# Optimization experiments

Measured on AMD Instinct MI355X. Metric: run time of the kernel, lower is better.

Reference implementation:

```python
import jax, jax.numpy as jnp
import numpy as np

EPS = 1e-15
BN_EPS = 1e-5
N_NODES = 50000
N_EDGES = 800000
IN_CH = 32
OUT_CH = 32
DIM = 3


def _gmm_params(key, in_ch, out_ch, K):
    k1, k2, k3, k4 = jax.random.split(key, 4)
    g = jax.random.normal(k1, (in_ch, K * out_ch), jnp.float32) * (1.0 / np.sqrt(in_ch))
    mu = jax.random.normal(k2, (K, DIM), jnp.float32)
    sigma = jax.random.uniform(k3, (K, DIM), jnp.float32, 0.5, 1.5)
    root = jax.random.normal(k4, (in_ch, out_ch), jnp.float32) * (1.0 / np.sqrt(in_ch))
    bias = jnp.zeros((out_ch,), jnp.float32)
    return g, mu, sigma, root, bias


def setup_inputs() -> dict:
    key = jax.random.key(0)
    ks = jax.random.split(key, 12)
    x = jax.random.normal(ks[0], (N_NODES, IN_CH), jnp.float32)
    edge_index = jax.random.randint(ks[1], (2, N_EDGES), 0, N_NODES, jnp.int64)
    edge_attr = jax.random.uniform(ks[2], (N_EDGES, DIM), jnp.float32)
    g1, mu1, sig1, root1, b1 = _gmm_params(ks[3], IN_CH, OUT_CH, 5)
    g2, mu2, sig2, root2, b2 = _gmm_params(ks[4], OUT_CH, OUT_CH, 5)
    gs, mus, sigs, roots, bs = _gmm_params(ks[5], IN_CH, OUT_CH, 1)
    ones = jnp.ones((OUT_CH,), jnp.float32)
    zeros = jnp.zeros((OUT_CH,), jnp.float32)
    return dict(x=x, edge_attr=edge_attr,
                g1=g1, mu1=mu1, sig1=sig1, root1=root1, b1=b1, gam1=ones, bet1=zeros,
                g2=g2, mu2=mu2, sig2=sig2, root2=root2, b2=b2, gam2=ones, bet2=zeros,
                gs=gs, mus=mus, sigs=sigs, roots=roots, bs=bs, gams=ones, bets=zeros,
                edge_index=edge_index)


def gmm_conv(x, edge_index, edge_attr, g, mu, sigma, root, bias, num_nodes):
    # PyG GMMConv (separate kernels=False, aggr='mean', root_weight=True)
    src, dst = edge_index[0], edge_index[1]
    K = mu.shape[0]
    out_ch = root.shape[1]
    # Gaussian mixture weights per edge/kernel: [E, K]
    diff = edge_attr[:, None, :] - mu[None, :, :]               # [E, K, D]
    w = jnp.exp(jnp.sum(-0.5 * diff * diff / (EPS + sigma[None] ** 2), axis=-1))
    # Project and gather source features: [E, K, out]
    xj = (x @ g).reshape(-1, K, out_ch)[src] if False else (x[src] @ g).reshape(-1, K, out_ch)
    msg = jnp.einsum('ek,ekc->ec', w, xj)                        # [E, out]
    agg = jax.ops.segment_sum(msg, dst, num_segments=num_nodes)
    cnt = jax.ops.segment_sum(jnp.ones((msg.shape[0],), msg.dtype), dst, num_segments=num_nodes)
    agg = agg / jnp.maximum(cnt, 1.0)[:, None]                   # mean aggregation
    return agg + x @ root + bias


def batch_norm(x, gamma, beta):
    mean = jnp.mean(x, axis=0)
    var = jnp.var(x, axis=0)
    return gamma * (x - mean) * jax.lax.rsqrt(var + BN_EPS) + beta


def reference(x, edge_attr,
              g1, mu1, sig1, root1, b1, gam1, bet1,
              g2, mu2, sig2, root2, b2, gam2, bet2,
              gs, mus, sigs, roots, bs, gams, bets,
              edge_index):
    n = x.shape[0]
    h = jax.nn.elu(batch_norm(gmm_conv(x, edge_index, edge_attr, g1, mu1, sig1, root1, b1, n), gam1, bet1))
    h = batch_norm(gmm_conv(h, edge_index, edge_attr, g2, mu2, sig2, root2, b2, n), gam2, bet2)
    s = batch_norm(gmm_conv(x, edge_index, edge_attr, gs, mus, sigs, roots, bs, n), gams, bets)
    return jax.nn.elu(h + s)
```

## Files before the change

### kernel.cpp

```cpp
#include <hip/hip_runtime.h>
#include <hip/hip_fp16.h>
#include <math.h>

#define NN 50000
#define NE 800000
#define GEPS 1e-15f
#define BN_EPS 1e-5f
#define NB 196
#define LOG2E 1.4426950408889634f
#define NODES_PER_XCD 6250

typedef _Float16 f16x8 __attribute__((ext_vector_type(8)));
typedef float f32x4 __attribute__((ext_vector_type(4)));

__device__ __forceinline__ float2 h2f(unsigned int u) {
    __half2 h = *reinterpret_cast<const __half2*>(&u);
    return __half22float2(h);
}

__global__ void precompute_gc(const float* __restrict__ sig1, const float* __restrict__ mu1,
                              const float* __restrict__ sig2, const float* __restrict__ mu2,
                              const float* __restrict__ sigs, const float* __restrict__ mus,
                              float* __restrict__ gc) {
    int s = threadIdx.x;
    if (s >= 11) return;
    const float* sg; const float* mu;
    if (s < 5)       { sg = sig1 + s * 3;       mu = mu1 + s * 3; }
    else if (s < 10) { sg = sig2 + (s - 5) * 3; mu = mu2 + (s - 5) * 3; }
    else             { sg = sigs;               mu = mus; }
    float C = 0.f;
    for (int d = 0; d < 3; d++) {
        float sv = sg[d];
        float iv = -0.5f / (GEPS + sv * sv) * LOG2E;
        float m = mu[d];
        gc[s * 8 + d] = iv;
        gc[s * 8 + 3 + d] = -2.f * iv * m;
        C += iv * m * m;
    }
    gc[s * 8 + 6] = C;
    gc[s * 8 + 7] = 0.f;
}

__global__ void rank_kernel(const int* __restrict__ ei, int* __restrict__ deg,
                            int* __restrict__ rankv) {
    int t = blockIdx.x * blockDim.x + threadIdx.x;
    int e0 = t * 4;
    if (e0 >= NE) return;
    int4 dv = *(const int4*)(ei + NE + e0);
    int4 rv;
    rv.x = atomicAdd(&deg[dv.x], 1);
    rv.y = atomicAdd(&deg[dv.y], 1);
    rv.z = atomicAdd(&deg[dv.z], 1);
    rv.w = atomicAdd(&deg[dv.w], 1);
    *(int4*)(rankv + e0) = rv;
}

__global__ void block_reduce_kernel(const int* __restrict__ deg, int* __restrict__ bsum) {
    __shared__ int sh[256];
    int t = threadIdx.x;
    int i = blockIdx.x * 256 + t;
    sh[t] = (i < NN) ? deg[i] : 0;
    __syncthreads();
    for (int off = 128; off > 0; off >>= 1) {
        if (t < off) sh[t] += sh[t + off];
        __syncthreads();
    }
    if (t == 0) bsum[blockIdx.x] = sh[0];
}

__global__ void scan_partials_kernel(int* __restrict__ bsum) {
    __shared__ int sh[256];
    int t = threadIdx.x;
    int v = (t < NB) ? bsum[t] : 0;
    sh[t] = v;
    __syncthreads();
    for (int off = 1; off < 256; off <<= 1) {
        int u = (t >= off) ? sh[t - off] : 0;
        __syncthreads();
        sh[t] += u;
        __syncthreads();
    }
    if (t < NB) bsum[t] = sh[t] - v;
}

__global__ void block_scan_kernel(const int* __restrict__ deg, const int* __restrict__ bsum,
                                  int* __restrict__ rowstart) {
    __shared__ int sh[256];
    int t = threadIdx.x;
    int i = blockIdx.x * 256 + t;
    int v = (i < NN) ? deg[i] : 0;
    sh[t] = v;
    __syncthreads();
    for (int off = 1; off < 256; off <<= 1) {
        int u = (t >= off) ? sh[t - off] : 0;
        __syncthreads();
        sh[t] += u;
        __syncthreads();
    }
    int excl = sh[t] - v + bsum[blockIdx.x];
    if (i < NN) rowstart[i] = excl;
}

__global__ void scatter_xcd(const int* __restrict__ ei, const int* __restrict__ rankv,
                            const int* __restrict__ rowstart, int* __restrict__ perm) {
    const int g = blockIdx.x & 7;
    const int v = blockIdx.x >> 3;
    const int VB = gridDim.x >> 3;
    const int stride = VB * blockDim.x * 4;
    for (int e0 = (v * blockDim.x + threadIdx.x) * 4; e0 < NE; e0 += stride) {
        int4 dv = *(const int4*)(ei + NE + e0);
        int4 rv = *(const int4*)(rankv + e0);
        if (dv.x / NODES_PER_XCD == g) perm[rowstart[dv.x] + rv.x] = e0;
        if (dv.y / NODES_PER_XCD == g) perm[rowstart[dv.y] + rv.y] = e0 + 1;
        if (dv.z / NODES_PER_XCD == g) perm[rowstart[dv.z] + rv.z] = e0 + 2;
        if (dv.w / NODES_PER_XCD == g) perm[rowstart[dv.w] + rv.w] = e0 + 3;
    }
}

__global__ void reorder_build(const int* __restrict__ perm, const int* __restrict__ ei,
                              const float* __restrict__ ea, const float* __restrict__ gc,
                              int4* __restrict__ recA, int4* __restrict__ recB) {
    int t = blockIdx.x * blockDim.x + threadIdx.x;
    int p0 = t * 4;
    if (p0 >= NE) return;
    int4 pv = *(const int4*)(perm + p0);
    int es[4] = {pv.x, pv.y, pv.z, pv.w};

    int   srcs[4];
    float av[4][3];
#pragma unroll
    for (int k = 0; k < 4; k++) {
        int e = es[k];
        srcs[k] = ei[e];
        av[k][0] = ea[e * 3 + 0];
        av[k][1] = ea[e * 3 + 1];
        av[k][2] = ea[e * 3 + 2];
    }

    int4 qa[4], qb[4];
#pragma unroll
    for (int k = 0; k < 4; k++) {
        float a0 = av[k][0], a1 = av[k][1], a2 = av[k][2];
        float s0 = a0 * a0, s1 = a1 * a1, s2 = a2 * a2;
        __half wv[11];
#pragma unroll
        for (int s = 0; s < 11; s++) {
            float ex = gc[s * 8 + 6];
            ex = fmaf(gc[s * 8 + 3], a0, ex);
            ex = fmaf(gc[s * 8 + 4], a1, ex);
            ex = fmaf(gc[s * 8 + 5], a2, ex);
            ex = fmaf(gc[s * 8 + 0], s0, ex);
            ex = fmaf(gc[s * 8 + 1], s1, ex);
            ex = fmaf(gc[s * 8 + 2], s2, ex);
            wv[s] = __float2half(exp2f(ex));
        }
        union UA { struct { int src; __half w[6]; } r; int4 q; } ua;
        ua.r.src = srcs[k];
        ua.r.w[0] = wv[0]; ua.r.w[1] = wv[1]; ua.r.w[2] = wv[2];
        ua.r.w[3] = wv[3]; ua.r.w[4] = wv[4]; ua.r.w[5] = wv[10];
        union UB { struct { int src; __half w[5]; __half pad; } r; int4 q; } ub;
        ub.r.src = srcs[k];
        ub.r.w[0] = wv[5]; ub.r.w[1] = wv[6]; ub.r.w[2] = wv[7];
        ub.r.w[3] = wv[8]; ub.r.w[4] = wv[9]; ub.r.pad = __float2half(0.f);
        qa[k] = ua.q;
        qb[k] = ub.q;
    }
#pragma unroll
    for (int k = 0; k < 4; k++) recA[p0 + k] = qa[k];
#pragma unroll
    for (int k = 0; k < 4; k++) recB[p0 + k] = qb[k];
}

__global__ void projR_kernel(const float* __restrict__ x, const float* __restrict__ root1,
                             const float* __restrict__ b1, const float* __restrict__ roots,
                             const float* __restrict__ bs, __half* __restrict__ xh,
                             float* __restrict__ R1, float* __restrict__ Rs) {
    const int t = threadIdx.x;
    const int col = t & 31;
    const int half_ = (t >> 5) & 1;
    const int rg = t >> 6;
    float w[32];
    const float* rootp = half_ ? roots : root1;
#pragma unroll
    for (int i = 0; i < 32; i++) w[i] = rootp[i * 32 + col];
    float b = half_ ? bs[col] : b1[col];
    float* Rp = half_ ? Rs : R1;
    __shared__ float hs[256];
    for (int n0 = blockIdx.x * 8; n0 < NN; n0 += gridDim.x * 8) {
        float v = x[(size_t)n0 * 32 + t];
        hs[t] = v;
        xh[(size_t)n0 * 32 + t] = __float2half(v);
        __syncthreads();
#pragma unroll
        for (int rr = 0; rr < 2; rr++) {
            int r = rg * 2 + rr;
            float acc = b;
#pragma unroll
            for (int i = 0; i < 32; i++) acc += w[i] * hs[r * 32 + i];
            Rp[(size_t)(n0 + r) * 32 + col] = acc;
        }
        __syncthreads();
    }
}

__global__ void projB2_kernel(const float* __restrict__ c1, const float* __restrict__ stats,
                              const float* __restrict__ gam1, const float* __restrict__ bet1,
                              const float* __restrict__ root2, const float* __restrict__ b2,
                              __half* __restrict__ hh, float* __restrict__ R2) {
    const int t = threadIdx.x;
    const int col = t & 31;
    const int rg = t >> 5;
    __shared__ float sc[32], sf[32];
    if (t < 32) {
        const float invN = 1.0f / (float)NN;
        float m = stats[t] * invN;
        float v = stats[32 + t] * invN - m * m;
        float s = gam1[t] * rsqrtf(v + BN_EPS);
        sc[t] = s;
        sf[t] = bet1[t] - m * s;
    }
    float w[32];
#pragma unroll
    for (int i = 0; i < 32; i++) w[i] = root2[i * 32 + col];
    float b = b2[col];
    __shared__ float hs[256];
    __syncthreads();
    for (int n0 = blockIdx.x * 8; n0 < NN; n0 += gridDim.x * 8) {
        float v = c1[(size_t)n0 * 32 + t];
        float hv = sc[t & 31] * v + sf[t & 31];
        hv = hv > 0.f ? hv : (__expf(hv) - 1.f);
        hs[t] = hv;
        hh[(size_t)n0 * 32 + t] = __float2half(hv);
        __syncthreads();
        float acc = b;
#pragma unroll
        for (int i = 0; i < 32; i++) acc += w[i] * hs[rg * 32 + i];
        R2[(size_t)(n0 + rg) * 32 + col] = acc;
        __syncthreads();
    }
}

template <bool SKIP>
__global__ void agg_kernel(const int4* __restrict__ rec, const int* __restrict__ rowstart,
                           const int* __restrict__ deg, const __half* __restrict__ X,
                           __half* __restrict__ Aout) {
    constexpr int NS = SKIP ? 6 : 5;
    constexpr int SA = SKIP ? 192 : 160;
    const int tid = blockIdx.x * blockDim.x + threadIdx.x;
    const int lane = threadIdx.x & 63;
    const int grp = lane >> 4;
    const int ch2 = lane & 15;
    const int wavesTotal = (gridDim.x * blockDim.x) >> 6;
    const int wid = tid >> 6;

    for (int n = wid; n < NN; n += wavesTotal) {
        const int start = rowstart[n];
        const int d = deg[n];
        float2 acc[NS];
#pragma unroll
        for (int s = 0; s < NS; s++) acc[s] = make_float2(0.f, 0.f);
        int i = grp;
        for (; i + 4 < d; i += 8) {
            int4 r0 = rec[(size_t)(start + i)];
            int4 r1 = rec[(size_t)(start + i + 4)];
            const __half2 xv0 = *(const __half2*)(X + (((size_t)r0.x) << 5) + 2 * ch2);
            const __half2 xv1 = *(const __half2*)(X + (((size_t)r1.x) << 5) + 2 * ch2);
            float2 xf0 = __half22float2(xv0);
            float2 xf1 = __half22float2(xv1);
            {
                float2 w01 = h2f((unsigned)r0.y);
                float2 w23 = h2f((unsigned)r0.z);
                float2 w45 = h2f((unsigned)r0.w);
                float wv[6] = {w01.x, w01.y, w23.x, w23.y, w45.x, w45.y};
#pragma unroll
                for (int s = 0; s < NS; s++) {
                    acc[s].x = fmaf(wv[s], xf0.x, acc[s].x);
                    acc[s].y = fmaf(wv[s], xf0.y, acc[s].y);
                }
            }
            {
                float2 w01 = h2f((unsigned)r1.y);
                float2 w23 = h2f((unsigned)r1.z);
                float2 w45 = h2f((unsigned)r1.w);
                float wv[6] = {w01.x, w01.y, w23.x, w23.y, w45.x, w45.y};
#pragma unroll
                for (int s = 0; s < NS; s++) {
                    acc[s].x = fmaf(wv[s], xf1.x, acc[s].x);
                    acc[s].y = fmaf(wv[s], xf1.y, acc[s].y);
                }
            }
        }
        if (i < d) {
            int4 r = rec[(size_t)(start + i)];
            const __half2 xv = *(const __half2*)(X + (((size_t)r.x) << 5) + 2 * ch2);
            float2 xf = __half22float2(xv);
            float2 w01 = h2f((unsigned)r.y);
            float2 w23 = h2f((unsigned)r.z);
            float2 w45 = h2f((unsigned)r.w);
            float wv[6] = {w01.x, w01.y, w23.x, w23.y, w45.x, w45.y};
#pragma unroll
            for (int s = 0; s < NS; s++) {
                acc[s].x = fmaf(wv[s], xf.x, acc[s].x);
                acc[s].y = fmaf(wv[s], xf.y, acc[s].y);
            }
        }
#pragma unroll
        for (int s = 0; s < NS; s++) {
            acc[s].x += __shfl_xor(acc[s].x, 16, 64);
            acc[s].x += __shfl_xor(acc[s].x, 32, 64);
            acc[s].y += __shfl_xor(acc[s].y, 16, 64);
            acc[s].y += __shfl_xor(acc[s].y, 32, 64);
        }
        if (grp == 0) {
            const float invd = 1.0f / fmaxf((float)d, 1.0f);
            __half* base = Aout + (size_t)n * SA + 2 * ch2;
#pragma unroll
            for (int s = 0; s < 5; s++) {
                __half2 hv = __floats2half2_rn(acc[s].x * invd, acc[s].y * invd);
                *(__half2*)(base + s * 32) = hv;
            }
            if (SKIP) {
                __half2 hv = __floats2half2_rn(acc[5].x * invd, acc[5].y * invd);
                *(__half2*)(base + 160) = hv;
            }
        }
    }
}

template <bool SKIP>
__global__ __launch_bounds__(256, 4) void gemm_kernel(
        const __half* __restrict__ Ah, const float* __restrict__ G,
        const float* __restrict__ Gs, const float* __restrict__ R,
        const float* __restrict__ Rs, float* __restrict__ C,
        float* __restrict__ Cs, float* __restrict__ stats) {
    constexpr int SA = SKIP ? 192 : 160;
    const int tid = blockIdx.x * blockDim.x + threadIdx.x;
    const int l = threadIdx.x & 63;
    const int r16 = l & 15;
    const int quad = l >> 4;
    const int wid = tid >> 6;
    const int nw = (gridDim.x * blockDim.x) >> 6;

    f16x8 bf[5][2];
#pragma unroll
    for (int kt = 0; kt < 5; kt++)
#pragma unroll
        for (int ct = 0; ct < 2; ct++)
#pragma unroll
            for (int e = 0; e < 8; e++) {
                int jj = quad * 8 + e;
                bf[kt][ct][e] = (_Float16)G[jj * 160 + kt * 32 + ct * 16 + r16];
            }
    f16x8 bs[2];
    if (SKIP) {
#pragma unroll
        for (int ct = 0; ct < 2; ct++)
#pragma unroll
            for (int e = 0; e < 8; e++) {
                int jj = quad * 8 + e;
                bs[ct][e] = (_Float16)Gs[jj * 32 + ct * 16 + r16];
            }
    }

    float s0 = 0.f, s1 = 0.f, q0 = 0.f, q1 = 0.f;
    float t0 = 0.f, t1 = 0.f, u0 = 0.f, u1 = 0.f;

    for (int tile = wid; tile < NN / 16; tile += nw) {
        const int n0 = tile * 16;
        const __half* arow = Ah + (size_t)(n0 + r16) * SA + quad * 8;
        f32x4 acc0 = {0.f, 0.f, 0.f, 0.f};
        f32x4 acc1 = {0.f, 0.f, 0.f, 0.f};
        f32x4 sa0 = {0.f, 0.f, 0.f, 0.f};
        f32x4 sa1 = {0.f, 0.f, 0.f, 0.f};
#pragma unroll
        for (int kt = 0; kt < 5; kt++) {
            f16x8 a = *(const f16x8*)(arow + kt * 32);
            acc0 = __builtin_amdgcn_mfma_f32_16x16x32_f16(a, bf[kt][0], acc0, 0, 0, 0);
            acc1 = __builtin_amdgcn_mfma_f32_16x16x32_f16(a, bf[kt][1], acc1, 0, 0, 0);
        }
        if (SKIP) {
            f16x8 a = *(const f16x8*)(arow + 160);
            sa0 = __builtin_amdgcn_mfma_f32_16x16x32_f16(a, bs[0], sa0, 0, 0, 0);
            sa1 = __builtin_amdgcn_mfma_f32_16x16x32_f16(a, bs[1], sa1, 0, 0, 0);
        }
#pragma unroll
        for (int r = 0; r < 4; r++) {
            const int nr = n0 + quad * 4 + r;
            const int b = nr * 32;
            {
                float v = acc0[r] + R[b + r16];
                C[b + r16] = v; s0 += v; q0 += v * v;
            }
            {
                float v = acc1[r] + R[b + 16 + r16];
                C[b + 16 + r16] = v; s1 += v; q1 += v * v;
            }
            if (SKIP) {
                float v = sa0[r] + Rs[b + r16];
                Cs[b + r16] = v; t0 += v; u0 += v * v;
                float w2 = sa1[r] + Rs[b + 16 + r16];
                Cs[b + 16 + r16] = w2; t1 += w2; u1 += w2 * w2;
            }
        }
    }
    s0 += __shfl_xor(s0, 16, 64); s0 += __shfl_xor(s0, 32, 64);
    s1 += __shfl_xor(s1, 16, 64); s1 += __shfl_xor(s1, 32, 64);
    q0 += __shfl_xor(q0, 16, 64); q0 += __shfl_xor(q0, 32, 64);
    q1 += __shfl_xor(q1, 16, 64); q1 += __shfl_xor(q1, 32, 64);
    if (SKIP) {
        t0 += __shfl_xor(t0, 16, 64); t0 += __shfl_xor(t0, 32, 64);
        t1 += __shfl_xor(t1, 16, 64); t1 += __shfl_xor(t1, 32, 64);
        u0 += __shfl_xor(u0, 16, 64); u0 += __shfl_xor(u0, 32, 64);
        u1 += __shfl_xor(u1, 16, 64); u1 += __shfl_xor(u1, 32, 64);
    }
    __shared__ float sred[128];
    const int t = threadIdx.x;
    if (t < 128) sred[t] = 0.f;
    __syncthreads();
    if (l < 16) {
        atomicAdd(&sred[l], s0);       atomicAdd(&sred[16 + l], s1);
        atomicAdd(&sred[32 + l], q0);  atomicAdd(&sred[48 + l], q1);
        if (SKIP) {
            atomicAdd(&sred[64 + l], t0);  atomicAdd(&sred[80 + l], t1);
            atomicAdd(&sred[96 + l], u0);  atomicAdd(&sred[112 + l], u1);
        }
    }
    __syncthreads();
    if (SKIP) { if (t < 128) atomicAdd(&stats[t], sred[t]); }
    else      { if (t < 64)  atomicAdd(&stats[t], sred[t]); }
}

__global__ void apply2_kernel(const float* __restrict__ c2, const float* __restrict__ cs,
                              const float* __restrict__ stats, const float* __restrict__ gam2,
                              const float* __restrict__ bet2, const float* __restrict__ gams,
                              const float* __restrict__ bets, float* __restrict__ out) {
    int idx = blockIdx.x * blockDim.x + threadIdx.x;
    if (idx >= NN * 32) return;
    int ch = idx & 31;
    const float invN = 1.0f / (float)NN;
    float m2 = stats[128 + ch] * invN;
    float v2 = stats[160 + ch] * invN - m2 * m2;
    float ms = stats[64 + ch] * invN;
    float vs = stats[96 + ch] * invN - ms * ms;
    float bn2 = gam2[ch] * (c2[idx] - m2) * rsqrtf(v2 + BN_EPS) + bet2[ch];
    float bns = gams[ch] * (cs[idx] - ms) * rsqrtf(vs + BN_EPS) + bets[ch];
    float o = bn2 + bns;
    out[idx] = o > 0.f ? o : (__expf(o) - 1.f);
}

extern "C" void kernel_launch(void* const* d_in, const int* in_sizes, int n_in,
                              void* d_out, int out_size, void* d_ws, size_t ws_size,
                              hipStream_t stream) {
    const float* x     = (const float*)d_in[0];
    const float* ea    = (const float*)d_in[1];
    const float* g1    = (const float*)d_in[2];
    const float* mu1   = (const float*)d_in[3];
    const float* sig1  = (const float*)d_in[4];
    const float* root1 = (const float*)d_in[5];
    const float* b1    = (const float*)d_in[6];
    const float* gam1  = (const float*)d_in[7];
    const float* bet1  = (const float*)d_in[8];
    const float* g2    = (const float*)d_in[9];
    const float* mu2   = (const float*)d_in[10];
    const float* sig2  = (const float*)d_in[11];
    const float* root2 = (const float*)d_in[12];
    const float* b2    = (const float*)d_in[13];
    const float* gam2  = (const float*)d_in[14];
    const float* bet2  = (const float*)d_in[15];
    const float* gs    = (const float*)d_in[16];
    const float* mus   = (const float*)d_in[17];
    const float* sigs  = (const float*)d_in[18];
    const float* roots = (const float*)d_in[19];
    const float* bs    = (const float*)d_in[20];
    const float* gams  = (const float*)d_in[21];
    const float* bets  = (const float*)d_in[22];
    const int*   ei    = (const int*)d_in[23];
    float* out = (float*)d_out;

    char* w = (char*)d_ws;
    __half* xh  = (__half*)w;   w += (size_t)NN * 32 * 2;
    __half* hh  = (__half*)w;   w += (size_t)NN * 32 * 2;
    __half* Ah  = (__half*)w;   w += (size_t)NN * 192 * 2;
    float*  R1  = (float*)w;    w += (size_t)NN * 32 * 4;
    float*  Rs  = (float*)w;    w += (size_t)NN * 32 * 4;
    float*  R2  = (float*)w;    w += (size_t)NN * 32 * 4;
    float*  c1  = (float*)w;    w += (size_t)NN * 32 * 4;
    float*  cs  = (float*)w;    w += (size_t)NN * 32 * 4;
    int4*   recA = (int4*)w;    w += (size_t)NE * 16;
    int4*   recB = (int4*)w;    w += (size_t)NE * 16;
    int*    perm = (int*)w;     w += (size_t)NE * 4;
    int*    rankv = (int*)w;    w += (size_t)NE * 4;
    int*    deg = (int*)w;      w += (size_t)NN * 4;
    int*    rowstart = (int*)w; w += (size_t)NN * 4;
    int*    bsum = (int*)w;     w += 256 * 4;
    float*  stats = (float*)w;  w += 256 * 4;
    float*  gc    = (float*)w;  w += 11 * 8 * 4;

    const int ilpBlocks   = (NE / 4 + 255) / 256;
    const int applyBlocks = (NN * 32 + 255) / 256;

    hipMemsetAsync(deg, 0, NN * sizeof(int), stream);
    hipMemsetAsync(stats, 0, 256 * sizeof(float), stream);
    precompute_gc<<<1, 16, 0, stream>>>(sig1, mu1, sig2, mu2, sigs, mus, gc);

    rank_kernel<<<ilpBlocks, 256, 0, stream>>>(ei, deg, rankv);
    block_reduce_kernel<<<NB, 256, 0, stream>>>(deg, bsum);
    scan_partials_kernel<<<1, 256, 0, stream>>>(bsum);
    block_scan_kernel<<<NB, 256, 0, stream>>>(deg, bsum, rowstart);
    scatter_xcd<<<1024, 256, 0, stream>>>(ei, rankv, rowstart, perm);
    reorder_build<<<ilpBlocks, 256, 0, stream>>>(perm, ei, ea, gc, recA, recB);

    projR_kernel<<<1024, 256, 0, stream>>>(x, root1, b1, roots, bs, xh, R1, Rs);
    agg_kernel<true><<<2048, 256, 0, stream>>>(recA, rowstart, deg, xh, Ah);
    gemm_kernel<true><<<512, 256, 0, stream>>>(Ah, g1, gs, R1, Rs, c1, cs, stats);

    projB2_kernel<<<1024, 256, 0, stream>>>(c1, stats, gam1, bet1, root2, b2, hh, R2);
    agg_kernel<false><<<2048, 256, 0, stream>>>(recB, rowstart, deg, hh, Ah);
    gemm_kernel<false><<<512, 256, 0, stream>>>(Ah, g2, nullptr, R2, nullptr, c1, nullptr,
                                                stats + 128);
    apply2_kernel<<<applyBlocks, 256, 0, stream>>>(c1, cs, stats, gam2, bet2, gams, bets, out);
}
```

Before: 303.3 us.

## Fuse edge aggregation and MFMA GEMM into one kernel via LDS tiles

Merges the aggregation kernel and the GEMM kernel so each block aggregates two 16-node tiles into shared memory and immediately runs the MFMA projection from LDS. This removes the global round trip of the aggregated Ah buffer and one launch per layer. In exchange, each block reloads G into shared memory, only half the waves do MFMA work, the grid becomes ~1563 short blocks, and the larger LDS footprint may reduce occupancy.

```diff
diff --git a/kernel.cpp b/kernel.cpp
--- a/kernel.cpp
+++ b/kernel.cpp
@@ -241,133 +241,133 @@
 }
 
 template <bool SKIP>
-__global__ void agg_kernel(const int4* __restrict__ rec, const int* __restrict__ rowstart,
-                           const int* __restrict__ deg, const __half* __restrict__ X,
-                           __half* __restrict__ Aout) {
+__global__ void aggemm_kernel(const int4* __restrict__ rec, const int* __restrict__ rowstart,
+                              const int* __restrict__ deg, const __half* __restrict__ X,
+                              const float* __restrict__ G, const float* __restrict__ Gs,
+                              const float* __restrict__ R, const float* __restrict__ Rs,
+                              float* __restrict__ C, float* __restrict__ Cs,
+                              float* __restrict__ stats) {
     constexpr int NS = SKIP ? 6 : 5;
-    constexpr int SA = SKIP ? 192 : 160;
-    const int tid = blockIdx.x * blockDim.x + threadIdx.x;
-    const int lane = threadIdx.x & 63;
+    constexpr int NM = SKIP ? 12 : 10;
+    constexpr int SAP = SKIP ? 200 : 168;
+    __shared__ alignas(16) __half At[2][16 * SAP];
+    __shared__ alignas(16) _Float16 Bl[NM][64][8];
+    __shared__ float sred[128];
+
+    const int t = threadIdx.x;
+    const int wv = t >> 6;
+    const int lane = t & 63;
     const int grp = lane >> 4;
     const int ch2 = lane & 15;
-    const int wavesTotal = (gridDim.x * blockDim.x) >> 6;
-    const int wid = tid >> 6;
-
-    for (int n = wid; n < NN; n += wavesTotal) {
-        const int start = rowstart[n];
-        const int d = deg[n];
-        float2 acc[NS];
-#pragma unroll
-        for (int s = 0; s < NS; s++) acc[s] = make_float2(0.f, 0.f);
-        int i = grp;
-        for (; i + 4 < d; i += 8) {
-            int4 r0 = rec[(size_t)(start + i)];
-            int4 r1 = rec[(size_t)(start + i + 4)];
-            const __half2 xv0 = *(const __half2*)(X + (((size_t)r0.x) << 5) + 2 * ch2);
-            const __half2 xv1 = *(const __half2*)(X + (((size_t)r1.x) << 5) + 2 * ch2);
-            float2 xf0 = __half22float2(xv0);
-            float2 xf1 = __half22float2(xv1);
-            {
-                float2 w01 = h2f((unsigned)r0.y);
-                float2 w23 = h2f((unsigned)r0.z);
-                float2 w45 = h2f((unsigned)r0.w);
-                float wv[6] = {w01.x, w01.y, w23.x, w23.y, w45.x, w45.y};
+    const int tl = wv >> 1;
+    const int half8 = wv & 1;
+    const int tileIdx = blockIdx.x * 2 + tl;
+    const bool tileOK = tileIdx < (NN / 16);
+    const int n0 = tileIdx * 16;
+
+    for (int idx = t; idx < NM * 64 * 8; idx += 256) {
+        int m = idx >> 9;
+        int rem = idx & 511;
+        int ln = rem >> 3;
+        int e = rem & 7;
+        int q_ = ln >> 4, r_ = ln & 15;
+        float v;
+        if (m < 10) {
+            int kt = m >> 1, ct = m & 1;
+            v = G[(q_ * 8 + e) * 160 + kt * 32 + ct * 16 + r_];
+        } else {
+            int ct = m - 10;
+            v = Gs[(q_ * 8 + e) * 32 + ct * 16 + r_];
+        }
+        Bl[m][ln][e] = (_Float16)v;
+    }
+    if (t < 128) sred[t] = 0.f;
+    __syncthreads();
+
+    if (tileOK) {
+        const int nbase = n0 + half8 * 8;
+        for (int nn = 0; nn < 8; nn++) {
+            const int n = nbase + nn;
+            const int start = rowstart[n];
+            const int d = deg[n];
+            float2 acc[NS];
+#pragma unroll
+            for (int s = 0; s < NS; s++) acc[s] = make_float2(0.f, 0.f);
+            int i = grp;
+            for (; i + 4 < d; i += 8) {
+                int4 r0 = rec[(size_t)(start + i)];
+                int4 r1 = rec[(size_t)(start + i + 4)];
+                const __half2 xv0 = *(const __half2*)(X + (((size_t)r0.x) << 5) + 2 * ch2);
+                const __half2 xv1 = *(const __half2*)(X + (((size_t)r1.x) << 5) + 2 * ch2);
+                float2 xf0 = __half22float2(xv0);
+                float2 xf1 = __half22float2(xv1);
+                {
+                    float2 w01 = h2f((unsigned)r0.y);
+                    float2 w23 = h2f((unsigned)r0.z);
+                    float2 w45 = h2f((unsigned)r0.w);
+                    float wvv[6] = {w01.x, w01.y, w23.x, w23.y, w45.x, w45.y};
+#pragma unroll
+                    for (int s = 0; s < NS; s++) {
+                        acc[s].x = fmaf(wvv[s], xf0.x, acc[s].x);
+                        acc[s].y = fmaf(wvv[s], xf0.y, acc[s].y);
+                    }
+                }
+                {
+                    float2 w01 = h2f((unsigned)r1.y);
+                    float2 w23 = h2f((unsigned)r1.z);
+                    float2 w45 = h2f((unsigned)r1.w);
+                    float wvv[6] = {w01.x, w01.y, w23.x, w23.y, w45.x, w45.y};
+#pragma unroll
+                    for (int s = 0; s < NS; s++) {
+                        acc[s].x = fmaf(wvv[s], xf1.x, acc[s].x);
+                        acc[s].y = fmaf(wvv[s], xf1.y, acc[s].y);
+                    }
+                }
+            }
+            if (i < d) {
+                int4 r = rec[(size_t)(start + i)];
+                const __half2 xv = *(const __half2*)(X + (((size_t)r.x) << 5) + 2 * ch2);
+                float2 xf = __half22float2(xv);
+                float2 w01 = h2f((unsigned)r.y);
+                float2 w23 = h2f((unsigned)r.z);
+                float2 w45 = h2f((unsigned)r.w);
+                float wvv[6] = {w01.x, w01.y, w23.x, w23.y, w45.x, w45.y};
 #pragma unroll
                 for (int s = 0; s < NS; s++) {
-                    acc[s].x = fmaf(wv[s], xf0.x, acc[s].x);
-                    acc[s].y = fmaf(wv[s], xf0.y, acc[s].y);
+                    acc[s].x = fmaf(wvv[s], xf.x, acc[s].x);
+                    acc[s].y = fmaf(wvv[s], xf.y, acc[s].y);
                 }
             }
-            {
-                float2 w01 = h2f((unsigned)r1.y);
-                float2 w23 = h2f((unsigned)r1.z);
-                float2 w45 = h2f((unsigned)r1.w);
-                float wv[6] = {w01.x, w01.y, w23.x, w23.y, w45.x, w45.y};
-#pragma unroll
-                for (int s = 0; s < NS; s++) {
-                    acc[s].x = fmaf(wv[s], xf1.x, acc[s].x);
-                    acc[s].y = fmaf(wv[s], xf1.y, acc[s].y);
+#pragma unroll
+            for (int s = 0; s < NS; s++) {
+                acc[s].x += __shfl_xor(acc[s].x, 16, 64);
+                acc[s].x += __shfl_xor(acc[s].x, 32, 64);
+                acc[s].y += __shfl_xor(acc[s].y, 16, 64);
+                acc[s].y += __shfl_xor(acc[s].y, 32, 64);
+            }
+            if (grp == 0) {
+                const float invd = 1.0f / fmaxf((float)d, 1.0f);
+                __half* base = &At[tl][(half8 * 8 + nn) * SAP + 2 * ch2];
+#pragma unroll
+                for (int s = 0; s < 5; s++) {
+                    *(__half2*)(base + s * 32) =
+                        __floats2half2_rn(acc[s].x * invd, acc[s].y * invd);
                 }
-            }
-        }
-        if (i < d) {
-            int4 r = rec[(size_t)(start + i)];
-            const __half2 xv = *(const __half2*)(X + (((size_t)r.x) << 5) + 2 * ch2);
-            float2 xf = __half22float2(xv);
-            float2 w01 = h2f((unsigned)r.y);
-            float2 w23 = h2f((unsigned)r.z);
-            float2 w45 = h2f((unsigned)r.w);
-            float wv[6] = {w01.x, w01.y, w23.x, w23.y, w45.x, w45.y};
-#pragma unroll
-            for (int s = 0; s < NS; s++) {
-                acc[s].x = fmaf(wv[s], xf.x, acc[s].x);
-                acc[s].y = fmaf(wv[s], xf.y, acc[s].y);
-            }
-        }
-#pragma unroll
-        for (int s = 0; s < NS; s++) {
-            acc[s].x += __shfl_xor(acc[s].x, 16, 64);
-            acc[s].x += __shfl_xor(acc[s].x, 32, 64);
-            acc[s].y += __shfl_xor(acc[s].y, 16, 64);
-            acc[s].y += __shfl_xor(acc[s].y, 32, 64);
-        }
-        if (grp == 0) {
-            const float invd = 1.0f / fmaxf((float)d, 1.0f);
-            __half* base = Aout + (size_t)n * SA + 2 * ch2;
-#pragma unroll
-            for (int s = 0; s < 5; s++) {
-                __half2 hv = __floats2half2_rn(acc[s].x * invd, acc[s].y * invd);
-                *(__half2*)(base + s * 32) = hv;
-            }
-            if (SKIP) {
-                __half2 hv = __floats2half2_rn(acc[5].x * invd, acc[5].y * invd);
-                *(__half2*)(base + 160) = hv;
-            }
-        }
-    }
-}
-
-template <bool SKIP>
-__global__ __launch_bounds__(256, 4) void gemm_kernel(
-        const __half* __restrict__ Ah, const float* __restrict__ G,
-        const float* __restrict__ Gs, const float* __restrict__ R,
-        const float* __restrict__ Rs, float* __restrict__ C,
-        float* __restrict__ Cs, float* __restrict__ stats) {
-    constexpr int SA = SKIP ? 192 : 160;
-    const int tid = blockIdx.x * blockDim.x + threadIdx.x;
-    const int l = threadIdx.x & 63;
-    const int r16 = l & 15;
-    const int quad = l >> 4;
-    const int wid = tid >> 6;
-    const int nw = (gridDim.x * blockDim.x) >> 6;
-
-    f16x8 bf[5][2];
-#pragma unroll
-    for (int kt = 0; kt < 5; kt++)
-#pragma unroll
-        for (int ct = 0; ct < 2; ct++)
-#pragma unroll
-            for (int e = 0; e < 8; e++) {
-                int jj = quad * 8 + e;
-                bf[kt][ct][e] = (_Float16)G[jj * 160 + kt * 32 + ct * 16 + r16];
-            }
-    f16x8 bs[2];
-    if (SKIP) {
-#pragma unroll
-        for (int ct = 0; ct < 2; ct++)
-#pragma unroll
-            for (int e = 0; e < 8; e++) {
-                int jj = quad * 8 + e;
-                bs[ct][e] = (_Float16)Gs[jj * 32 + ct * 16 + r16];
-            }
-    }
+                if (SKIP) {
+                    *(__half2*)(base + 160) =
+                        __floats2half2_rn(acc[5].x * invd, acc[5].y * invd);
+                }
+            }
+        }
+    }
+    __syncthreads();
 
     float s0 = 0.f, s1 = 0.f, q0 = 0.f, q1 = 0.f;
     float t0 = 0.f, t1 = 0.f, u0 = 0.f, u1 = 0.f;
-
-    for (int tile = wid; tile < NN / 16; tile += nw) {
-        const int n0 = tile * 16;
-        const __half* arow = Ah + (size_t)(n0 + r16) * SA + quad * 8;
+    if (tileOK && half8 == 0) {
+        const int r16 = ch2;
+        const int quad = grp;
+        const __half* arow = &At[tl][r16 * SAP + quad * 8];
         f32x4 acc0 = {0.f, 0.f, 0.f, 0.f};
         f32x4 acc1 = {0.f, 0.f, 0.f, 0.f};
         f32x4 sa0 = {0.f, 0.f, 0.f, 0.f};
@@ -375,13 +375,17 @@
 #pragma unroll
         for (int kt = 0; kt < 5; kt++) {
             f16x8 a = *(const f16x8*)(arow + kt * 32);
-            acc0 = __builtin_amdgcn_mfma_f32_16x16x32_f16(a, bf[kt][0], acc0, 0, 0, 0);
-            acc1 = __builtin_amdgcn_mfma_f32_16x16x32_f16(a, bf[kt][1], acc1, 0, 0, 0);
+            f16x8 b0 = *(const f16x8*)&Bl[kt * 2][lane][0];
+            f16x8 b1 = *(const f16x8*)&Bl[kt * 2 + 1][lane][0];
+            acc0 = __builtin_amdgcn_mfma_f32_16x16x32_f16(a, b0, acc0, 0, 0, 0);
+            acc1 = __builtin_amdgcn_mfma_f32_16x16x32_f16(a, b1, acc1, 0, 0, 0);
         }
         if (SKIP) {
             f16x8 a = *(const f16x8*)(arow + 160);
-            sa0 = __builtin_amdgcn_mfma_f32_16x16x32_f16(a, bs[0], sa0, 0, 0, 0);
-            sa1 = __builtin_amdgcn_mfma_f32_16x16x32_f16(a, bs[1], sa1, 0, 0, 0);
+            f16x8 b0 = *(const f16x8*)&Bl[NM - 2][lane][0];
+            f16x8 b1 = *(const f16x8*)&Bl[NM - 1][lane][0];
+            sa0 = __builtin_amdgcn_mfma_f32_16x16x32_f16(a, b0, sa0, 0, 0, 0);
+            sa1 = __builtin_amdgcn_mfma_f32_16x16x32_f16(a, b1, sa1, 0, 0, 0);
         }
 #pragma unroll
         for (int r = 0; r < 4; r++) {
@@ -413,16 +417,12 @@
         u0 += __shfl_xor(u0, 16, 64); u0 += __shfl_xor(u0, 32, 64);
         u1 += __shfl_xor(u1, 16, 64); u1 += __shfl_xor(u1, 32, 64);
     }
-    __shared__ float sred[128];
-    const int t = threadIdx.x;
-    if (t < 128) sred[t] = 0.f;
-    __syncthreads();
-    if (l < 16) {
-        atomicAdd(&sred[l], s0);       atomicAdd(&sred[16 + l], s1);
-        atomicAdd(&sred[32 + l], q0);  atomicAdd(&sred[48 + l], q1);
+    if (lane < 16) {
+        atomicAdd(&sred[lane], s0);       atomicAdd(&sred[16 + lane], s1);
+        atomicAdd(&sred[32 + lane], q0);  atomicAdd(&sred[48 + lane], q1);
         if (SKIP) {
-            atomicAdd(&sred[64 + l], t0);  atomicAdd(&sred[80 + l], t1);
-            atomicAdd(&sred[96 + l], u0);  atomicAdd(&sred[112 + l], u1);
+            atomicAdd(&sred[64 + lane], t0);  atomicAdd(&sred[80 + lane], t1);
+            atomicAdd(&sred[96 + lane], u0);  atomicAdd(&sred[112 + lane], u1);
         }
     }
     __syncthreads();
@@ -480,7 +480,6 @@
     char* w = (char*)d_ws;
     __half* xh  = (__half*)w;   w += (size_t)NN * 32 * 2;
     __half* hh  = (__half*)w;   w += (size_t)NN * 32 * 2;
-    __half* Ah  = (__half*)w;   w += (size_t)NN * 192 * 2;
     float*  R1  = (float*)w;    w += (size_t)NN * 32 * 4;
     float*  Rs  = (float*)w;    w += (size_t)NN * 32 * 4;
     float*  R2  = (float*)w;    w += (size_t)NN * 32 * 4;
@@ -498,6 +497,7 @@
 
     const int ilpBlocks   = (NE / 4 + 255) / 256;
     const int applyBlocks = (NN * 32 + 255) / 256;
+    const int fusedBlocks = (NN / 16 + 1) / 2;
 
     hipMemsetAsync(deg, 0, NN * sizeof(int), stream);
     hipMemsetAsync(stats, 0, 256 * sizeof(float), stream);
@@ -511,12 +511,12 @@
     reorder_build<<<ilpBlocks, 256, 0, stream>>>(perm, ei, ea, gc, recA, recB);
 
     projR_kernel<<<1024, 256, 0, stream>>>(x, root1, b1, roots, bs, xh, R1, Rs);
-    agg_kernel<true><<<2048, 256, 0, stream>>>(recA, rowstart, deg, xh, Ah);
-    gemm_kernel<true><<<512, 256, 0, stream>>>(Ah, g1, gs, R1, Rs, c1, cs, stats);
+    aggemm_kernel<true><<<fusedBlocks, 256, 0, stream>>>(recA, rowstart, deg, xh, g1, gs,
+                                                         R1, Rs, c1, cs, stats);
 
     projB2_kernel<<<1024, 256, 0, stream>>>(c1, stats, gam1, bet1, root2, b2, hh, R2);
-    agg_kernel<false><<<2048, 256, 0, stream>>>(recB, rowstart, deg, hh, Ah);
-    gemm_kernel<false><<<512, 256, 0, stream>>>(Ah, g2, nullptr, R2, nullptr, c1, nullptr,
-                                                stats + 128);
+    aggemm_kernel<false><<<fusedBlocks, 256, 0, stream>>>(recB, rowstart, deg, hh, g2, nullptr,
+                                                          R2, nullptr, c1, nullptr,
+                                                          stats + 128);
     apply2_kernel<<<applyBlocks, 256, 0, stream>>>(c1, cs, stats, gam2, bet2, gams, bets, out);
 }
```

Result: slower. 349.6 us (+15.3%).
